# Kernel tuning notes

Hardware: AMD Instinct MI355X
Metric: run time of the kernel (lower is better)

The kernel has to match this reference:

```python
import jax, jax.numpy as jnp
import numpy as np

N, L, S, D = 2, 4800, 4800, 256
H0, W0, H1, W1 = 60, 80, 60, 80  # hw0_c, hw1_c (L = H0*W0, S = H1*W1)
THR = 0.2
TEMP = 0.1           # dsmax_temperature
BORDER = 2           # border_rm
INF = 1e9


def setup_inputs() -> dict:
    key = jax.random.key(0)
    k0, k1, k2, k3 = jax.random.split(key, 4)
    feat_c0 = jax.random.normal(k0, (N, L, D), jnp.float32)
    feat_c1 = jax.random.normal(k1, (N, S, D), jnp.float32)
    # final_proj params (Linear(256, 256, bias=True)); scaled like typical init
    W = jax.random.normal(k2, (D, D), jnp.float32) / np.sqrt(D)
    b = jax.random.normal(k3, (D,), jnp.float32) * 0.01
    mask_c0 = jnp.ones((N, L), dtype=bool)
    mask_c1 = jnp.ones((N, S), dtype=bool)
    return {"feat_c0": feat_c0, "feat_c1": feat_c1, "W": W, "b": b,
            "mask_c0": mask_c0, "mask_c1": mask_c1}


def _border_valid(h, w, bd):
    # flattened (h*w,) bool: True away from all four borders (mask_border with v=False)
    r = jnp.arange(h * w)
    hh, ww = r // w, r % w
    return (hh >= bd) & (hh < h - bd) & (ww >= bd) & (ww < w - bd)


def reference(feat_c0, feat_c1, W, b, mask_c0, mask_c1):
    inv_sqrt_d = 1.0 / jnp.sqrt(jnp.asarray(D, jnp.float32))
    # final_proj + 1/sqrt(C) scaling
    f0 = (feat_c0 @ W.T + b) * inv_sqrt_d   # [N, L, D]
    f1 = (feat_c1 @ W.T + b) * inv_sqrt_d   # [N, S, D]
    # pairwise similarity / temperature, masked_fill(-INF) on padded pairs
    sim = jnp.einsum('nlc,nsc->nls', f0, f1) / TEMP   # [N, L, S]
    valid = mask_c0[:, :, None] & mask_c1[:, None, :]
    sim = jnp.where(valid, sim, -INF)
    # dual softmax
    conf_0_to_1 = jax.nn.softmax(sim, axis=2)
    conf_1_to_0 = jax.nn.softmax(sim, axis=1)
    # mutual nearest-neighbour + threshold mask
    m01 = (conf_0_to_1 > THR) & (conf_0_to_1 == conf_0_to_1.max(axis=2, keepdims=True))
    m10 = (conf_1_to_0 > THR) & (conf_1_to_0 == conf_1_to_0.max(axis=1, keepdims=True))
    match_mask = m01 | m10
    # border removal (mask_border with v=False on the [b,h0,w0,h1,w1] view)
    match_mask = (match_mask
                  & _border_valid(H0, W0, BORDER)[None, :, None]
                  & _border_valid(H1, W1, BORDER)[None, None, :])
    # dense form of mconf = max(conf01, conf10) at selected matches
    mconf = jnp.maximum(conf_0_to_1, conf_1_to_0) * match_mask
    return conf_0_to_1, conf_1_to_0, match_mask, mconf
```

## Files before the change

### kernel.cpp

```cpp
#include <hip/hip_runtime.h>

#define LL   4800
#define SSZ  4800
#define DD   256
#define LP   4864
#define NBAT 2

typedef __bf16 bf16x8 __attribute__((ext_vector_type(8)));
typedef float  f32x4  __attribute__((ext_vector_type(4)));

__device__ __forceinline__ unsigned short f2bf(float x) {
  unsigned u = __float_as_uint(x);
  u += 0x7FFFu + ((u >> 16) & 1u);
  return (unsigned short)(u >> 16);
}
__device__ __forceinline__ float bf2f(unsigned short h) {
  return __uint_as_float(((unsigned)h) << 16);
}
__device__ __forceinline__ void gl_lds16(const void* g, void* lds) {
  __builtin_amdgcn_global_load_lds(
      (const __attribute__((address_space(1))) void*)g,
      (__attribute__((address_space(3))) void*)lds, 16, 0, 0);
}
__device__ __forceinline__ bool border_ok(int idx) {
  const int h = idx / 80, w = idx % 80;
  return (h >= 2) && (h < 58) && (w >= 2) && (w < 78);
}

__global__ void k_convert(const float* __restrict__ in,
                          unsigned short* __restrict__ hi,
                          unsigned short* __restrict__ lo, int n4) {
  int i = blockIdx.x * blockDim.x + threadIdx.x;
  if (i >= n4) return;
  float4 v = reinterpret_cast<const float4*>(in)[i];
  float xs[4] = {v.x, v.y, v.z, v.w};
  unsigned short hs[4], ls[4];
#pragma unroll
  for (int j = 0; j < 4; ++j) {
    unsigned short h = f2bf(xs[j]);
    hs[j] = h;
    ls[j] = f2bf(xs[j] - bf2f(h));
  }
  ushort4 ho; ho.x = hs[0]; ho.y = hs[1]; ho.z = hs[2]; ho.w = hs[3];
  ushort4 lov; lov.x = ls[0]; lov.y = ls[1]; lov.z = ls[2]; lov.w = ls[3];
  reinterpret_cast<ushort4*>(hi)[i] = ho;
  reinterpret_cast<ushort4*>(lo)[i] = lov;
}

__global__ __launch_bounds__(256, 2)
void k_gemm_proj(const unsigned short* __restrict__ fc0hi, const unsigned short* __restrict__ fc0lo,
                 const unsigned short* __restrict__ fc1hi, const unsigned short* __restrict__ fc1lo,
                 const unsigned short* __restrict__ Whi,  const unsigned short* __restrict__ Wlo,
                 const float* __restrict__ bias,
                 unsigned short* __restrict__ f0h, unsigned short* __restrict__ f1h) {
  extern __shared__ unsigned char smem[];
  unsigned char* sAhi = smem;
  unsigned char* sAlo = smem + 16384;
  unsigned char* sBhi = smem + 32768;
  unsigned char* sBlo = smem + 49152;

  const int t = threadIdx.x;
  const int lane = t & 63, wave = t >> 6;
  const int wr = wave >> 1, wc = wave & 1;
  const int l15 = lane & 15, g4 = lane >> 4;
  const int tr = t >> 3, tch = t & 7;
  const int chg = tch ^ (tr & 7);

  const int mtile = blockIdx.x, ntile = blockIdx.y, tz = blockIdx.z;
  const int nb = (mtile >= 38) ? 1 : 0;
  const int ltile = mtile - nb * 38;

  const unsigned short* Fhi = tz ? fc1hi : fc0hi;
  const unsigned short* Flo = tz ? fc1lo : fc0lo;
  unsigned short* Oh = tz ? f1h : f0h;

  f32x4 acc[4][4] = {};

  for (int kt = 0; kt < DD / 64; ++kt) {
#pragma unroll
    for (int i = 0; i < 4; ++i) {
      const int r = i * 32 + tr;
      const int lrow = ltile * 128 + r;
      const int srcRow = nb * LL + min(lrow, LL - 1);
      const size_t aoff = (size_t)srcRow * DD + kt * 64 + chg * 8;
      const size_t boff = (size_t)(ntile * 128 + r) * DD + kt * 64 + chg * 8;
      const int ldsoff = i * 4096 + t * 16;
      gl_lds16(Fhi + aoff, sAhi + ldsoff);
      gl_lds16(Flo + aoff, sAlo + ldsoff);
      gl_lds16(Whi + boff, sBhi + ldsoff);
      gl_lds16(Wlo + boff, sBlo + ldsoff);
    }
    __syncthreads();
#pragma unroll
    for (int kk = 0; kk < 2; ++kk) {
      bf16x8 ah[4], al[4], bh[4], bl[4];
#pragma unroll
      for (int m = 0; m < 4; ++m) {
        const int r = wr * 64 + m * 16 + l15;
        const int off = r * 128 + (((kk * 4 + g4) ^ (r & 7)) * 16);
        ah[m] = *reinterpret_cast<const bf16x8*>(sAhi + off);
        al[m] = *reinterpret_cast<const bf16x8*>(sAlo + off);
      }
#pragma unroll
      for (int n = 0; n < 4; ++n) {
        const int r = wc * 64 + n * 16 + l15;
        const int off = r * 128 + (((kk * 4 + g4) ^ (r & 7)) * 16);
        bh[n] = *reinterpret_cast<const bf16x8*>(sBhi + off);
        bl[n] = *reinterpret_cast<const bf16x8*>(sBlo + off);
      }
#pragma unroll
      for (int m = 0; m < 4; ++m)
#pragma unroll
        for (int n = 0; n < 4; ++n) {
          acc[m][n] = __builtin_amdgcn_mfma_f32_16x16x32_bf16(ah[m], bh[n], acc[m][n], 0, 0, 0);
          acc[m][n] = __builtin_amdgcn_mfma_f32_16x16x32_bf16(ah[m], bl[n], acc[m][n], 0, 0, 0);
          acc[m][n] = __builtin_amdgcn_mfma_f32_16x16x32_bf16(al[m], bh[n], acc[m][n], 0, 0, 0);
        }
    }
    __syncthreads();
  }

#pragma unroll
  for (int m = 0; m < 4; ++m) {
#pragma unroll
    for (int j = 0; j < 4; ++j) {
      const int lrow = ltile * 128 + wr * 64 + m * 16 + g4 * 4 + j;
      const bool v = lrow < LL;
#pragma unroll
      for (int n = 0; n < 4; ++n) {
        const int dcol = ntile * 128 + wc * 64 + n * 16 + l15;
        float val = v ? (acc[m][n][j] + bias[dcol]) * 0.0625f : 0.0f;
        size_t oi = ((size_t)(nb * LP + lrow)) * DD + dcol;
        Oh[oi] = f2bf(val);
      }
    }
  }
}

__device__ __forceinline__ void sim_gemm(const unsigned short* __restrict__ Ah,
                                         const unsigned short* __restrict__ Bh,
                                         int bxs, int byl,
                                         unsigned char* sA, unsigned char* sB,
                                         f32x4 acc[4][4]) {
  const int t = threadIdx.x;
  const int lane = t & 63, wave = t >> 6;
  const int wr = wave >> 1, wc = wave & 1;
  const int l15 = lane & 15, g4 = lane >> 4;
  const int tr = t >> 3, tch = t & 7;
  const int chg = tch ^ (tr & 7);

  for (int kt = 0; kt < DD / 64; ++kt) {
#pragma unroll
    for (int i = 0; i < 4; ++i) {
      const int r = i * 32 + tr;
      const size_t aoff = (size_t)(byl * 128 + r) * DD + kt * 64 + chg * 8;
      const size_t boff = (size_t)(bxs * 128 + r) * DD + kt * 64 + chg * 8;
      const int ldsoff = i * 4096 + t * 16;
      gl_lds16(Ah + aoff, sA + ldsoff);
      gl_lds16(Bh + boff, sB + ldsoff);
    }
    __syncthreads();
#pragma unroll
    for (int kk = 0; kk < 2; ++kk) {
      bf16x8 ah[4], bh[4];
#pragma unroll
      for (int m = 0; m < 4; ++m) {
        const int r = wr * 64 + m * 16 + l15;
        const int off = r * 128 + (((kk * 4 + g4) ^ (r & 7)) * 16);
        ah[m] = *reinterpret_cast<const bf16x8*>(sA + off);
      }
#pragma unroll
      for (int n = 0; n < 4; ++n) {
        const int r = wc * 64 + n * 16 + l15;
        const int off = r * 128 + (((kk * 4 + g4) ^ (r & 7)) * 16);
        bh[n] = *reinterpret_cast<const bf16x8*>(sB + off);
      }
#pragma unroll
      for (int m = 0; m < 4; ++m)
#pragma unroll
        for (int n = 0; n < 4; ++n)
          acc[m][n] = __builtin_amdgcn_mfma_f32_16x16x32_bf16(ah[m], bh[n], acc[m][n], 0, 0, 0);
    }
    __syncthreads();
  }
}

__global__ __launch_bounds__(256, 2)
void k_sim_stats(const unsigned short* __restrict__ f0h, const unsigned short* __restrict__ f1h,
                 float* __restrict__ rowsum, float* __restrict__ colsum,
                 unsigned* __restrict__ rowmaxU, unsigned* __restrict__ colmaxU) {
  extern __shared__ unsigned char smem[];
  unsigned char* sA = smem;
  unsigned char* sB = smem + 16384;

  const int t = threadIdx.x;
  const int lane = t & 63, wave = t >> 6;
  const int wr = wave >> 1, wc = wave & 1;
  const int l15 = lane & 15, g4 = lane >> 4;

  const int bxs = blockIdx.x, byl = blockIdx.y, bz = blockIdx.z;
  const unsigned short* Ah = f0h + (size_t)bz * LP * DD;
  const unsigned short* Bh = f1h + (size_t)bz * LP * DD;

  f32x4 acc[4][4] = {};
  sim_gemm(Ah, Bh, bxs, byl, sA, sB, acc);

  bool colv[4];
#pragma unroll
  for (int n = 0; n < 4; ++n)
    colv[n] = (bxs * 128 + wc * 64 + n * 16 + l15) < SSZ;

#pragma unroll
  for (int m = 0; m < 4; ++m) {
#pragma unroll
    for (int j = 0; j < 4; ++j) {
      const int lg = byl * 128 + wr * 64 + m * 16 + g4 * 4 + j;
      const bool rowv = lg < LL;
#pragma unroll
      for (int n = 0; n < 4; ++n) {
        float p = __expf(acc[m][n][j] * 10.0f);
        if (!rowv || !colv[n]) p = 0.0f;
        acc[m][n][j] = p;
      }
    }
  }

  float* srow = (float*)smem;
  float* scol = srow + 128;
  unsigned* srm = (unsigned*)(scol + 128);
  unsigned* scm = srm + 128;
  __syncthreads();
  if (t < 128) { srow[t] = 0.f; scol[t] = 0.f; srm[t] = 0u; scm[t] = 0u; }
  __syncthreads();

#pragma unroll
  for (int m = 0; m < 4; ++m) {
#pragma unroll
    for (int j = 0; j < 4; ++j) {
      float s  = acc[m][0][j] + acc[m][1][j] + acc[m][2][j] + acc[m][3][j];
      float mx = fmaxf(fmaxf(acc[m][0][j], acc[m][1][j]), fmaxf(acc[m][2][j], acc[m][3][j]));
#pragma unroll
      for (int o = 1; o < 16; o <<= 1) {
        s += __shfl_xor(s, o);
        mx = fmaxf(mx, __shfl_xor(mx, o));
      }
      if (l15 == 0) {
        const int r = wr * 64 + m * 16 + g4 * 4 + j;
        atomicAdd(&srow[r], s);
        atomicMax(&srm[r], __float_as_uint(mx));
      }
    }
  }
#pragma unroll
  for (int n = 0; n < 4; ++n) {
    float s = 0.f, mx = 0.f;
#pragma unroll
    for (int m = 0; m < 4; ++m)
#pragma unroll
      for (int j = 0; j < 4; ++j) { s += acc[m][n][j]; mx = fmaxf(mx, acc[m][n][j]); }
    s += __shfl_xor(s, 16); mx = fmaxf(mx, __shfl_xor(mx, 16));
    s += __shfl_xor(s, 32); mx = fmaxf(mx, __shfl_xor(mx, 32));
    if (g4 == 0) {
      const int c = wc * 64 + n * 16 + l15;
      atomicAdd(&scol[c], s);
      atomicMax(&scm[c], __float_as_uint(mx));
    }
  }
  __syncthreads();

  if (t < 128) {
    const int lg = byl * 128 + t;
    if (lg < LL) {
      atomicAdd(&rowsum[bz * LL + lg], srow[t]);
      atomicMax(&rowmaxU[bz * LL + lg], srm[t]);
    }
    const int sg = bxs * 128 + t;
    if (sg < SSZ) {
      atomicAdd(&colsum[bz * SSZ + sg], scol[t]);
      atomicMax(&colmaxU[bz * SSZ + sg], scm[t]);
    }
  }
}

__global__ __launch_bounds__(256, 2)
void k_sim_write(const unsigned short* __restrict__ f0h, const unsigned short* __restrict__ f1h,
                 const float* __restrict__ rowsum, const float* __restrict__ colsum,
                 const unsigned* __restrict__ rowmaxU, const unsigned* __restrict__ colmaxU,
                 float* __restrict__ out0, float* __restrict__ out1,
                 float* __restrict__ out2, float* __restrict__ out3) {
  extern __shared__ unsigned char smem[];
  unsigned char* sA = smem;
  unsigned char* sB = smem + 16384;

  const int t = threadIdx.x;
  const int lane = t & 63, wave = t >> 6;
  const int wr = wave >> 1, wc = wave & 1;
  const int l15 = lane & 15, g4 = lane >> 4;

  const int bxs = blockIdx.x, byl = blockIdx.y, bz = blockIdx.z;
  const unsigned short* Ah = f0h + (size_t)bz * LP * DD;
  const unsigned short* Bh = f1h + (size_t)bz * LP * DD;

  f32x4 acc[4][4] = {};
  sim_gemm(Ah, Bh, bxs, byl, sA, sB, acc);

  int   sg[4];
  bool  colv[4], bs[4];
  float invcs[4], cpm[4];
#pragma unroll
  for (int n = 0; n < 4; ++n) {
    sg[n] = bxs * 128 + wc * 64 + n * 16 + l15;
    colv[n] = sg[n] < SSZ;
    const int c = colv[n] ? sg[n] : 0;
    invcs[n] = 1.0f / colsum[bz * SSZ + c];
    cpm[n]   = __uint_as_float(colmaxU[bz * SSZ + c]);
    bs[n]    = colv[n] && border_ok(sg[n]);
  }

#pragma unroll
  for (int m = 0; m < 4; ++m) {
#pragma unroll
    for (int j = 0; j < 4; ++j) {
      const int lg = byl * 128 + wr * 64 + m * 16 + g4 * 4 + j;
      if (lg >= LL) continue;
      const float invrs = 1.0f / rowsum[bz * LL + lg];
      const float rpm   = __uint_as_float(rowmaxU[bz * LL + lg]);
      const bool  bl    = border_ok(lg);
      const size_t rowoff = ((size_t)bz * LL + lg) * SSZ;
#pragma unroll
      for (int n = 0; n < 4; ++n) {
        if (!colv[n]) continue;
        const float p   = __expf(acc[m][n][j] * 10.0f);
        const float c01 = p * invrs;
        const float c10 = p * invcs[n];
        const bool m01 = (c01 > 0.2f) && (p >= rpm);
        const bool m10 = (c10 > 0.2f) && (p >= cpm[n]);
        const bool mm  = (m01 || m10) && bl && bs[n];
        out0[rowoff + sg[n]] = c01;
        out1[rowoff + sg[n]] = c10;
        out2[rowoff + sg[n]] = mm ? 1.0f : 0.0f;
        out3[rowoff + sg[n]] = mm ? fmaxf(c01, c10) : 0.0f;
      }
    }
  }
}

extern "C" void kernel_launch(void* const* d_in, const int* in_sizes, int n_in,
                              void* d_out, int out_size, void* d_ws, size_t ws_size,
                              hipStream_t stream) {
  const float* feat0 = (const float*)d_in[0];
  const float* feat1 = (const float*)d_in[1];
  const float* Wm    = (const float*)d_in[2];
  const float* bv    = (const float*)d_in[3];

  char* ws = (char*)d_ws;
  unsigned short* fc0hi = (unsigned short*)(ws + 0);
  unsigned short* fc0lo = (unsigned short*)(ws + 4915200);
  unsigned short* fc1hi = (unsigned short*)(ws + 9830400);
  unsigned short* fc1lo = (unsigned short*)(ws + 14745600);
  unsigned short* Whi   = (unsigned short*)(ws + 19660800);
  unsigned short* Wlo   = (unsigned short*)(ws + 19791872);
  unsigned short* f0h   = (unsigned short*)(ws + 19922944);
  unsigned short* f1h   = (unsigned short*)(ws + 24903680);
  char* statsBase = ws + 29884416;
  float*    rowsum  = (float*)(statsBase + 0);
  float*    colsum  = (float*)(statsBase + 38400);
  unsigned* rowmaxU = (unsigned*)(statsBase + 76800);
  unsigned* colmaxU = (unsigned*)(statsBase + 115200);

  const size_t NLS = (size_t)NBAT * LL * SSZ;
  float* out0 = (float*)d_out;
  float* out1 = out0 + NLS;
  float* out2 = out0 + 2 * NLS;
  float* out3 = out0 + 3 * NLS;

  hipMemsetAsync(statsBase, 0, 153600, stream);

  k_convert<<<2400, 256, 0, stream>>>(feat0, fc0hi, fc0lo, 614400);
  k_convert<<<2400, 256, 0, stream>>>(feat1, fc1hi, fc1lo, 614400);
  k_convert<<<64, 256, 0, stream>>>(Wm, Whi, Wlo, 16384);

  k_gemm_proj<<<dim3(76, 2, 2), 256, 65536, stream>>>(
      fc0hi, fc0lo, fc1hi, fc1lo, Whi, Wlo, bv, f0h, f1h);

  k_sim_stats<<<dim3(38, 38, 2), 256, 32768, stream>>>(
      f0h, f1h, rowsum, colsum, rowmaxU, colmaxU);

  k_sim_write<<<dim3(38, 38, 2), 256, 32768, stream>>>(
      f0h, f1h, rowsum, colsum, rowmaxU, colmaxU, out0, out1, out2, out3);
}
```

Baseline: 261.4 us.

## Merge convert launches, remap sim blocks per XCD, use nontemporal output stores

Three conversion launches are merged into one kernel that picks its source by global index. The sim kernels move to a 1D grid whose block IDs are remapped so each group of eight consecutive IDs (wgid mod 8) gets its own contiguous chunk of tiles, aiming at L2 locality on the multi-XCD MI355X. The four large output writes become nontemporal stores to avoid polluting the cache with streaming data. The main cost targeted is the write bandwidth of the ~740MB outputs, plus some launch overhead.

Result: slower. 327.5 us (+25.2%).

```diff
diff --git a/kernel.cpp b/kernel.cpp
--- a/kernel.cpp
+++ b/kernel.cpp
@@ -26,13 +26,30 @@
   const int h = idx / 80, w = idx % 80;
   return (h >= 2) && (h < 58) && (w >= 2) && (w < 78);
 }
-
-__global__ void k_convert(const float* __restrict__ in,
-                          unsigned short* __restrict__ hi,
-                          unsigned short* __restrict__ lo, int n4) {
+__device__ __forceinline__ void sim_block_decode(int wgid, int& bxs, int& byl, int& bz) {
+  const int logical = (wgid & 7) * 361 + (wgid >> 3);
+  bz = logical / 1444;
+  const int rem = logical - bz * 1444;
+  byl = rem / 38;
+  bxs = rem - byl * 38;
+}
+
+#define F4_FEAT 614400
+#define F4_TOT  (F4_FEAT * 2 + 16384)
+__global__ void k_convert_all(const float* __restrict__ f0, const float* __restrict__ f1,
+                              const float* __restrict__ Wm,
+                              unsigned short* __restrict__ fc0hi, unsigned short* __restrict__ fc0lo,
+                              unsigned short* __restrict__ fc1hi, unsigned short* __restrict__ fc1lo,
+                              unsigned short* __restrict__ Whi,  unsigned short* __restrict__ Wlo) {
   int i = blockIdx.x * blockDim.x + threadIdx.x;
-  if (i >= n4) return;
-  float4 v = reinterpret_cast<const float4*>(in)[i];
+  if (i >= F4_TOT) return;
+  const float* src;
+  unsigned short *hi, *lo;
+  int off;
+  if (i < F4_FEAT)          { src = f0; hi = fc0hi; lo = fc0lo; off = i; }
+  else if (i < 2 * F4_FEAT) { src = f1; hi = fc1hi; lo = fc1lo; off = i - F4_FEAT; }
+  else                      { src = Wm; hi = Whi;  lo = Wlo;  off = i - 2 * F4_FEAT; }
+  float4 v = reinterpret_cast<const float4*>(src)[off];
   float xs[4] = {v.x, v.y, v.z, v.w};
   unsigned short hs[4], ls[4];
 #pragma unroll
@@ -43,8 +60,8 @@
   }
   ushort4 ho; ho.x = hs[0]; ho.y = hs[1]; ho.z = hs[2]; ho.w = hs[3];
   ushort4 lov; lov.x = ls[0]; lov.y = ls[1]; lov.z = ls[2]; lov.w = ls[3];
-  reinterpret_cast<ushort4*>(hi)[i] = ho;
-  reinterpret_cast<ushort4*>(lo)[i] = lov;
+  reinterpret_cast<ushort4*>(hi)[off] = ho;
+  reinterpret_cast<ushort4*>(lo)[off] = lov;
 }
 
 __global__ __launch_bounds__(256, 2)
@@ -198,7 +215,8 @@
   const int wr = wave >> 1, wc = wave & 1;
   const int l15 = lane & 15, g4 = lane >> 4;
 
-  const int bxs = blockIdx.x, byl = blockIdx.y, bz = blockIdx.z;
+  int bxs, byl, bz;
+  sim_block_decode(blockIdx.x, bxs, byl, bz);
   const unsigned short* Ah = f0h + (size_t)bz * LP * DD;
   const unsigned short* Bh = f1h + (size_t)bz * LP * DD;
 
@@ -297,7 +315,8 @@
   const int wr = wave >> 1, wc = wave & 1;
   const int l15 = lane & 15, g4 = lane >> 4;
 
-  const int bxs = blockIdx.x, byl = blockIdx.y, bz = blockIdx.z;
+  int bxs, byl, bz;
+  sim_block_decode(blockIdx.x, bxs, byl, bz);
   const unsigned short* Ah = f0h + (size_t)bz * LP * DD;
   const unsigned short* Bh = f1h + (size_t)bz * LP * DD;
 
@@ -305,7 +324,7 @@
   sim_gemm(Ah, Bh, bxs, byl, sA, sB, acc);
 
   int   sg[4];
-  bool  colv[4], bs[4];
+  bool  colv[4], bsc[4];
   float invcs[4], cpm[4];
 #pragma unroll
   for (int n = 0; n < 4; ++n) {
@@ -314,7 +333,7 @@
     const int c = colv[n] ? sg[n] : 0;
     invcs[n] = 1.0f / colsum[bz * SSZ + c];
     cpm[n]   = __uint_as_float(colmaxU[bz * SSZ + c]);
-    bs[n]    = colv[n] && border_ok(sg[n]);
+    bsc[n]   = colv[n] && border_ok(sg[n]);
   }
 
 #pragma unroll
@@ -335,11 +354,11 @@
         const float c10 = p * invcs[n];
         const bool m01 = (c01 > 0.2f) && (p >= rpm);
         const bool m10 = (c10 > 0.2f) && (p >= cpm[n]);
-        const bool mm  = (m01 || m10) && bl && bs[n];
-        out0[rowoff + sg[n]] = c01;
-        out1[rowoff + sg[n]] = c10;
-        out2[rowoff + sg[n]] = mm ? 1.0f : 0.0f;
-        out3[rowoff + sg[n]] = mm ? fmaxf(c01, c10) : 0.0f;
+        const bool mm  = (m01 || m10) && bl && bsc[n];
+        __builtin_nontemporal_store(c01, &out0[rowoff + sg[n]]);
+        __builtin_nontemporal_store(c10, &out1[rowoff + sg[n]]);
+        __builtin_nontemporal_store(mm ? 1.0f : 0.0f, &out2[rowoff + sg[n]]);
+        __builtin_nontemporal_store(mm ? fmaxf(c01, c10) : 0.0f, &out3[rowoff + sg[n]]);
       }
     }
   }
@@ -376,16 +395,15 @@
 
   hipMemsetAsync(statsBase, 0, 153600, stream);
 
-  k_convert<<<2400, 256, 0, stream>>>(feat0, fc0hi, fc0lo, 614400);
-  k_convert<<<2400, 256, 0, stream>>>(feat1, fc1hi, fc1lo, 614400);
-  k_convert<<<64, 256, 0, stream>>>(Wm, Whi, Wlo, 16384);
+  k_convert_all<<<(F4_TOT + 255) / 256, 256, 0, stream>>>(
+      feat0, feat1, Wm, fc0hi, fc0lo, fc1hi, fc1lo, Whi, Wlo);
 
   k_gemm_proj<<<dim3(76, 2, 2), 256, 65536, stream>>>(
       fc0hi, fc0lo, fc1hi, fc1lo, Whi, Wlo, bv, f0h, f1h);
 
-  k_sim_stats<<<dim3(38, 38, 2), 256, 32768, stream>>>(
+  k_sim_stats<<<2888, 256, 32768, stream>>>(
       f0h, f1h, rowsum, colsum, rowmaxU, colmaxU);
 
-  k_sim_write<<<dim3(38, 38, 2), 256, 32768, stream>>>(
+  k_sim_write<<<2888, 256, 32768, stream>>>(
       f0h, f1h, rowsum, colsum, rowmaxU, colmaxU, out0, out1, out2, out3);
 }
```
